# Optimization experiments

Measured on AMD Instinct MI355X. Metric: run time of the kernel, lower is better.

## Reference

```python
import jax, jax.numpy as jnp
import numpy as np

B, S, D, H = 4, 2048, 512, 8
INNER = D  # assumed AttentionHead.inner_size == size (naive single-head attention)


def setup_inputs() -> dict:
    key = jax.random.key(0)
    ks = jax.random.split(key, 8)
    scale = 0.02
    return {
        "emb_input": jax.random.normal(ks[0], (B, S, D), dtype=jnp.float32),
        "Wq": jax.random.normal(ks[1], (H, D, INNER), dtype=jnp.float32) * scale,
        "bq": jnp.zeros((H, INNER), dtype=jnp.float32),
        "Wk": jax.random.normal(ks[2], (H, D, INNER), dtype=jnp.float32) * scale,
        "bk": jnp.zeros((H, INNER), dtype=jnp.float32),
        "Wv": jax.random.normal(ks[3], (H, D, INNER), dtype=jnp.float32) * scale,
        "bv": jnp.zeros((H, INNER), dtype=jnp.float32),
        "Wp": jax.random.normal(ks[4], (H * INNER, D), dtype=jnp.float32) * scale,
        "bp": jnp.zeros((D,), dtype=jnp.float32),
    }


def reference(emb_input, Wq, bq, Wk, bk, Wv, bv, Wp, bp):
    # All heads batched into one einsum instead of a Python loop over submodules.
    x = emb_input  # [B, S, D]
    q = jnp.einsum("bsd,hde->bhse", x, Wq) + bq[None, :, None, :]  # [B,H,S,E]
    k = jnp.einsum("bsd,hde->bhse", x, Wk) + bk[None, :, None, :]
    v = jnp.einsum("bsd,hde->bhse", x, Wv) + bv[None, :, None, :]
    scores = jnp.einsum("bhse,bhte->bhst", q, k) / jnp.sqrt(
        jnp.asarray(INNER, dtype=x.dtype)
    )  # [B,H,S,S]
    attn = jax.nn.softmax(scores, axis=-1)
    o = jnp.einsum("bhst,bhte->bhse", attn, v)  # [B,H,S,E]
    # concat over heads (dim=2 in torch => feature dim after per-head outputs)
    o = jnp.transpose(o, (0, 2, 1, 3)).reshape(B, S, H * INNER)
    return o @ Wp + bp  # [B, S, D]
```

## Files before the change

kernel.cpp:

```cpp
#include <hip/hip_runtime.h>


typedef short s8v __attribute__((ext_vector_type(8)));
typedef float f4v __attribute__((ext_vector_type(4)));
typedef unsigned short us;
typedef us us4v __attribute__((ext_vector_type(4)));

__device__ inline us f2b(float f) {
  union { float f; unsigned u; } v; v.f = f;
  unsigned r = v.u + 0x7FFFu + ((v.u >> 16) & 1u);
  return (us)(r >> 16);
}

__device__ inline void gld16(const us* g, us* l) {
  __builtin_amdgcn_global_load_lds(
      (const __attribute__((address_space(1))) void*)g,
      (__attribute__((address_space(3))) void*)l, 16, 0, 0);
}

__global__ __launch_bounds__(512, 2) void attn_fused(
    const us* __restrict__ Q, const us* __restrict__ Kh,
    const us* __restrict__ Vt, us* __restrict__ O,
    int Lh, float alpha) {
  constexpr int S = 2048, E = 512;
  constexpr int NCH = (S / 128) * 8;
  __shared__ __align__(16) us smem[66560];
  const int t = threadIdx.x, w = t >> 6, ln = t & 63;
  const int m16 = ln & 15, quad = ln >> 4;

  const int gx = gridDim.x;
  const int nblk = gx * gridDim.y;
  const int flat = blockIdx.x + gx * blockIdx.y;
  int nid = flat;
  if ((nblk & 7) == 0) nid = (flat & 7) * (nblk >> 3) + (flat >> 3);
  const int qt = nid % gx, zh = nid / gx;

  const long long zoff = (long long)zh * S * E;
  const us* Qz = Q + zoff;
  const us* Kz = Kh + zoff;
  const us* Vz = Vt + zoff;
  const int q0 = qt * 128;

  s8v Qf[16];
  {
    const us* qrow = Qz + (long long)(q0 + 16 * w + m16) * E + quad * 8;
#pragma unroll
    for (int kq = 0; kq < 16; ++kq) Qf[kq] = *(const s8v*)(qrow + kq * 32);
  }

  f4v accO[4][8];
#pragma unroll
  for (int e = 0; e < 4; ++e)
#pragma unroll
    for (int nb = 0; nb < 8; ++nb) accO[e][nb] = (f4v){0.f, 0.f, 0.f, 0.f};
  float la[4] = {0.f, 0.f, 0.f, 0.f};

#define STAGE(g_, sl_)                                                       \
  {                                                                          \
    const int tau_ = (g_) >> 3, sub_ = (g_) & 7;                             \
    us* dst_ = smem + (sl_) * 16384;                                         \
    _Pragma("unroll") for (int j = 0; j < 4; ++j) {                          \
      const int c_ = t + 512 * j;                                            \
      const int s_ = c_ >> 6, l_ = c_ & 63;                                  \
      const int nbm_ = ((s_ >> 2) * 16 + (l_ & 15));                         \
      const int kk_ = (s_ & 3) * 32 + (l_ >> 4) * 8;                         \
      const us* src_ = (sub_ < 4)                                            \
          ? Kz + (long long)(tau_ * 128 + nbm_) * E + sub_ * 128 + kk_       \
          : Vz + (long long)((sub_ - 4) * 128 + nbm_) * S + tau_ * 128 + kk_;\
      gld16(src_, dst_ + c_ * 8);                                            \
    }                                                                        \
  }

  STAGE(0, 0);
  STAGE(1, 1);
  STAGE(2, 2);
  int sl = 0;

  for (int tau = 0; tau < S / 128; ++tau) {
    f4v accS[8];
#pragma unroll
    for (int nb = 0; nb < 8; ++nb) accS[nb] = (f4v){0.f, 0.f, 0.f, 0.f};
    s8v pa[4];
#pragma unroll
    for (int ph = 0; ph < 8; ++ph) {
      const int g = tau * 8 + ph;
      const int slc = sl;
      if (g + 3 <= NCH)      asm volatile("s_waitcnt vmcnt(8)" ::: "memory");
      else if (g + 2 == NCH) asm volatile("s_waitcnt vmcnt(4)" ::: "memory");
      else                   asm volatile("s_waitcnt vmcnt(0)" ::: "memory");
      __builtin_amdgcn_s_barrier();
      const us* rb = smem + slc * 16384;
      __builtin_amdgcn_s_setprio(1);
#pragma unroll
      for (int ks = 0; ks < 4; ++ks) {
#pragma unroll
        for (int h = 0; h < 2; ++h) {
          s8v bf[4];
#pragma unroll
          for (int nb = 0; nb < 4; ++nb)
            bf[nb] = *(const s8v*)&rb[(((h * 4 + nb) * 4 + ks) * 64 + ln) * 8];
          if (ph < 4) {
#pragma unroll
            for (int nb = 0; nb < 4; ++nb)
              accS[h * 4 + nb] = __builtin_amdgcn_mfma_f32_16x16x32_bf16(
                  Qf[ph * 4 + ks], bf[nb], accS[h * 4 + nb], 0, 0, 0);
          } else {
#pragma unroll
            for (int nb = 0; nb < 4; ++nb)
              accO[ph - 4][h * 4 + nb] = __builtin_amdgcn_mfma_f32_16x16x32_bf16(
                  pa[ks], bf[nb], accO[ph - 4][h * 4 + nb], 0, 0, 0);
          }
        }
      }
      __builtin_amdgcn_s_setprio(0);
      __builtin_amdgcn_s_barrier();
      if (g + 3 < NCH) STAGE(g + 3, slc);
      if (ph == 3) {
        us* pw = smem + 49152 + w * 2176;
#pragma unroll
        for (int nb = 0; nb < 8; ++nb)
#pragma unroll
          for (int gg = 0; gg < 4; ++gg) {
            accS[nb][gg] = __expf(fmaf(accS[nb][gg], alpha, -4.f));
            pw[(quad * 4 + gg) * 136 + nb * 16 + m16] = f2b(accS[nb][gg]);
          }
#pragma unroll
        for (int gg = 0; gg < 4; ++gg) {
          float s = 0.f;
#pragma unroll
          for (int nb = 0; nb < 8; ++nb) s += accS[nb][gg];
          s += __shfl_xor(s, 1, 64);
          s += __shfl_xor(s, 2, 64);
          s += __shfl_xor(s, 4, 64);
          s += __shfl_xor(s, 8, 64);
          la[gg] += s;
        }
        asm volatile("s_waitcnt lgkmcnt(0)" ::: "memory");
        __builtin_amdgcn_sched_barrier(0);
#pragma unroll
        for (int kp = 0; kp < 4; ++kp)
          pa[kp] = *(const s8v*)&pw[m16 * 136 + kp * 32 + quad * 8];
      }
      sl = (slc == 2) ? 0 : slc + 1;
    }
  }
#undef STAGE

  float inv[4];
#pragma unroll
  for (int gg = 0; gg < 4; ++gg) inv[gg] = 1.f / la[gg];
  const int b = zh >> Lh, hc = zh & ((1 << Lh) - 1);
  const int HCE = E << Lh;
  us* Ob = O + (long long)b * S * HCE + (long long)hc * E;
  us* stw = smem + w * 4288;
#pragma unroll
  for (int half = 0; half < 2; ++half) {
#pragma unroll
    for (int ec = 0; ec < 2; ++ec) {
      const int ecg = half * 2 + ec;
#pragma unroll
      for (int nb = 0; nb < 8; ++nb)
#pragma unroll
        for (int gg = 0; gg < 4; ++gg)
          stw[(quad * 4 + gg) * 268 + ec * 128 + nb * 16 + m16] =
              f2b(accO[ecg][nb][gg] * inv[gg]);
    }
    asm volatile("s_waitcnt lgkmcnt(0)" ::: "memory");
    __builtin_amdgcn_sched_barrier(0);
#pragma unroll
    for (int rp = 0; rp < 8; ++rp) {
      const int row = rp * 2 + (ln >> 5);
      const s8v v = *(const s8v*)&stw[row * 268 + (ln & 31) * 8];
      __builtin_nontemporal_store(
          v, (s8v*)&Ob[(long long)(q0 + 16 * w + row) * HCE + half * 256 +
                       (ln & 31) * 8]);
    }
    if (half == 0) {
      asm volatile("s_waitcnt lgkmcnt(0)" ::: "memory");
      __builtin_amdgcn_sched_barrier(0);
    }
  }
}

template <int EPI>
__global__ __launch_bounds__(512, 2) void gemm_nt(
    const us* __restrict__ A, int lda, long long sA0, long long sA1,
    const us* __restrict__ Bm, int ldb, long long sB0, long long sB1,
    const float* __restrict__ bias, const float* __restrict__ bias2,
    const float* __restrict__ bias3,
    void* __restrict__ Cv, void* __restrict__ C2, void* __restrict__ C3,
    int ldc, long long sC0, long long sC1,
    int K, float alpha, int L, int sbits) {
  __shared__ __align__(16) us As[2][16384];
  __shared__ __align__(16) us Bs[2][16384];
  const int t = threadIdx.x;
  const int wv = t >> 6, ln = t & 63;
  const int m16 = ln & 15, quad = ln >> 4;

  const int gx = gridDim.x, gxy = gx * gridDim.y;
  const int nblk = gxy * gridDim.z;
  const int flat = blockIdx.x + gx * blockIdx.y + gxy * blockIdx.z;
  int nid = flat;
  if ((nblk & 7) == 0) nid = (flat & 7) * (nblk >> 3) + (flat >> 3);
  const int bz = nid / gxy, rem = nid % gxy;
  const int by = rem / gx, bx = rem % gx;

  const long long row0 = (long long)by * 256;
  const long long col0 = (long long)bx * 256;
  const int zo = bz >> L, zi = bz & ((1 << L) - 1);
  const us* Az = A + zo * sA0 + zi * sA1;
  const us* Bz = Bm + zo * sB0 + zi * sB1;

  int offA[4], offB[4];
#pragma unroll
  for (int j = 0; j < 4; ++j) {
    const int c = t + 512 * j;
    const int s = c >> 6, l = c & 63;
    const int mb = s >> 1, ks = s & 1, qd = (l >> 4) & 3, mm = l & 15;
    offA[j] = (int)((row0 + mb * 16 + mm) * (long long)lda + ks * 32 + qd * 8);
    offB[j] = (int)((col0 + mb * 16 + mm) * (long long)ldb + ks * 32 + qd * 8);
  }

  f4v acc[8][4];
#pragma unroll
  for (int r = 0; r < 8; ++r)
#pragma unroll
    for (int c = 0; c < 4; ++c) acc[r][c] = (f4v){0.f, 0.f, 0.f, 0.f};

  const int nk = K >> 6;
  const int wr = wv >> 2, wc = wv & 3;

#define BARR __builtin_amdgcn_s_barrier()
#define LGKM0                                              \
  do {                                                     \
    asm volatile("s_waitcnt lgkmcnt(0)" ::: "memory");     \
    __builtin_amdgcn_sched_barrier(0);                     \
  } while (0)
#define READ_A(p_)                                                           \
  _Pragma("unroll") for (int rr = 0; rr < 2; ++rr)                           \
  _Pragma("unroll") for (int ks = 0; ks < 2; ++ks)                           \
      af[rr * 2 + ks] = *(const s8v*)&As[b]                                  \
          [(((wr * 8 + (p_) * 2 + rr) * 2 + ks) * 64 + ln) * 8];
#define MFMA_Q(p_)                                                           \
  __builtin_amdgcn_s_setprio(1);                                             \
  _Pragma("unroll") for (int ks = 0; ks < 2; ++ks)                           \
  _Pragma("unroll") for (int rr = 0; rr < 2; ++rr)                           \
  _Pragma("unroll") for (int c = 0; c < 4; ++c)                              \
      acc[(p_) * 2 + rr][c] = __builtin_amdgcn_mfma_f32_16x16x32_bf16(       \
          af[rr * 2 + ks], bfr[c * 2 + ks], acc[(p_) * 2 + rr][c], 0, 0, 0); \
  __builtin_amdgcn_s_setprio(0);

#pragma unroll
  for (int j = 0; j < 4; ++j) gld16(Az + offA[j], (us*)As[0] + (t + 512 * j) * 8);
#pragma unroll
  for (int j = 0; j < 4; ++j) gld16(Bz + offB[j], (us*)Bs[0] + (t + 512 * j) * 8);
  if (nk > 1) {
#pragma unroll
    for (int j = 0; j < 4; ++j)
      gld16(Bz + offB[j] + 64, (us*)Bs[1] + (t + 512 * j) * 8);
    gld16(Az + offA[0] + 64, (us*)As[1] + t * 8);
    gld16(Az + offA[2] + 64, (us*)As[1] + (t + 1024) * 8);
    asm volatile("s_waitcnt vmcnt(6)" ::: "memory");
  } else {
    asm volatile("s_waitcnt vmcnt(0)" ::: "memory");
  }
  BARR;

  for (int kt = 0; kt < nk; ++kt) {
    const int b = kt & 1;
    s8v bfr[8], af[4];
#pragma unroll
    for (int c = 0; c < 4; ++c)
#pragma unroll
      for (int ks = 0; ks < 2; ++ks)
        bfr[c * 2 + ks] =
            *(const s8v*)&Bs[b][(((wc * 4 + c) * 2 + ks) * 64 + ln) * 8];
    READ_A(0);
    if (kt + 1 < nk) {
      const int kof = (kt + 1) << 6;
      gld16(Az + offA[1] + kof, (us*)As[b ^ 1] + (t + 512) * 8);
      gld16(Az + offA[3] + kof, (us*)As[b ^ 1] + (t + 1536) * 8);
    }
    asm volatile("s_waitcnt lgkmcnt(8)" ::: "memory");
    BARR; LGKM0; MFMA_Q(0); BARR;
    READ_A(1);
    if (kt + 2 < nk) {
      const int kof = (kt + 2) << 6;
#pragma unroll
      for (int j = 0; j < 4; ++j)
        gld16(Bz + offB[j] + kof, (us*)Bs[b] + (t + 512 * j) * 8);
    }
    BARR; LGKM0; MFMA_Q(1); BARR;
    READ_A(2);
    if (kt + 2 < nk) {
      const int kof = (kt + 2) << 6;
      gld16(Az + offA[0] + kof, (us*)As[b] + t * 8);
      gld16(Az + offA[2] + kof, (us*)As[b] + (t + 1024) * 8);
    }
    BARR; LGKM0; MFMA_Q(2); BARR;
    READ_A(3);
    BARR; LGKM0; MFMA_Q(3);
    if (kt + 2 < nk) asm volatile("s_waitcnt vmcnt(6)" ::: "memory");
    else             asm volatile("s_waitcnt vmcnt(0)" ::: "memory");
    BARR;
  }
#undef READ_A
#undef MFMA_Q
#undef BARR
#undef LGKM0

#pragma unroll
  for (int r = 0; r < 8; ++r) {
    const int inRow = wr * 128 + r * 16 + quad * 4;
    const long long gr0 = row0 + inRow;
#pragma unroll
    for (int c = 0; c < 4; ++c) {
      const long long gc = col0 + wc * 64 + c * 16 + m16;
      if (EPI == 3) {
        const int which = (int)(gc >> sbits);
        const int gsec = (int)gc & ((1 << sbits) - 1);
        const int hc = gsec >> 9, e = (int)gc & 511;
        const long long slice =
            ((long long)zo * (1 << (sbits - 9)) + hc) * 1048576LL;
        if (which == 0) {
          us* C = (us*)Cv;
          const float bb = bias[gsec];
#pragma unroll
          for (int g = 0; g < 4; ++g)
            __builtin_nontemporal_store(f2b(acc[r][c][g] + bb),
                                        &C[slice + (gr0 + g) * 512 + e]);
        } else if (which == 1) {
          us* C = (us*)C2;
          const float bb = bias2[gsec];
#pragma unroll
          for (int g = 0; g < 4; ++g)
            __builtin_nontemporal_store(f2b(acc[r][c][g] + bb),
                                        &C[slice + (gr0 + g) * 512 + e]);
        } else {
          us* C = (us*)C3;
          const float bb = bias3[gsec];
          us4v pk;
#pragma unroll
          for (int g = 0; g < 4; ++g) pk[g] = f2b(acc[r][c][g] + bb);
          __builtin_nontemporal_store(
              pk, (us4v*)&C[slice + (long long)e * 2048 + gr0]);
        }
      } else {
        float* C = (float*)Cv + zo * sC0;
        float* p = C + gr0 * ldc + gc;
#pragma unroll
        for (int g = 0; g < 4; ++g)
          atomicAdd(&p[(long long)g * ldc], acc[r][c][g] * alpha);
      }
    }
  }
}

__global__ __launch_bounds__(256) void conv_bf16(const float* __restrict__ in,
                                                 us* __restrict__ out, int n4) {
  const int i = blockIdx.x * 256 + threadIdx.x;
  if (i < n4) {
    const float4 f = ((const float4*)in)[i];
    us4v o;
    o[0] = f2b(f.x); o[1] = f2b(f.y); o[2] = f2b(f.z); o[3] = f2b(f.w);
    ((us4v*)out)[i] = o;
  }
}

__global__ __launch_bounds__(256) void conv_transpose(const float* __restrict__ in,
                                                      us* __restrict__ out,
                                                      int R, int C, int Lc,
                                                      int mask, long long sChunk) {
  __shared__ float tile[32][33];
  const int tx = threadIdx.x & 31, ty = threadIdx.x >> 5;
  const int z = blockIdx.z;
  const long long zi = (long long)z * R * C;
  us* dst = out + (long long)(z >> Lc) * sChunk + (long long)(z & mask) * R * C;
  const int r0 = blockIdx.y * 32, c0 = blockIdx.x * 32;
#pragma unroll
  for (int j = 0; j < 4; ++j)
    tile[ty + 8 * j][tx] = in[zi + (long long)(r0 + ty + 8 * j) * C + c0 + tx];
  __syncthreads();
#pragma unroll
  for (int j = 0; j < 4; ++j)
    dst[(long long)(c0 + ty + 8 * j) * R + r0 + tx] = f2b(tile[tx][ty + 8 * j]);
}

__global__ __launch_bounds__(256) void init_out_kernel(float* __restrict__ out,
                                                       const float* __restrict__ bp,
                                                       int total) {
  const int i = blockIdx.x * 256 + threadIdx.x;
  if (i < total) out[i] = bp[i & 511];
}

extern "C" void kernel_launch(void* const* d_in, const int* in_sizes, int n_in,
                              void* d_out, int out_size, void* d_ws, size_t ws_size,
                              hipStream_t stream) {
  constexpr int Bb = 4, S = 2048, D = 512, H = 8, E = 512, HE = 4096;
  const float* x  = (const float*)d_in[0];
  const float* Wq = (const float*)d_in[1];
  const float* bq = (const float*)d_in[2];
  const float* Wk = (const float*)d_in[3];
  const float* bk = (const float*)d_in[4];
  const float* Wv = (const float*)d_in[5];
  const float* bv = (const float*)d_in[6];
  const float* Wp = (const float*)d_in[7];
  const float* bp = (const float*)d_in[8];
  float* out = (float*)d_out;

  const long long SE = (long long)S * E;
  const long long SD = (long long)S * D, ED = (long long)E * D;

  us* xh  = (us*)d_ws;
  us* W3  = xh + 4194304;
  us* WpT = W3 + 6291456;
  us* dyn = WpT + 2097152;

  const size_t fixedB = (size_t)(4194304 + 6291456 + 2097152) * 2;
  int HC = 8;
  while (HC > 1) {
    const size_t need = fixedB + (size_t)4 * HC * Bb * SE * 2;
    if (need <= ws_size) break;
    HC >>= 1;
  }
  const int Lh = (HC == 8) ? 3 : (HC == 4) ? 2 : (HC == 2) ? 1 : 0;
  const int BHC = Bb * HC;
  const int sbits = 9 + Lh;

  us* qh = dyn;
  us* kh = qh + (size_t)BHC * SE;
  us* vT = kh + (size_t)BHC * SE;
  us* oh = vT + (size_t)BHC * SE;

  const dim3 tb(256), tg(512);
  init_out_kernel<<<dim3((Bb * S * D + 255) / 256), tb, 0, stream>>>(
      out, bp, Bb * S * D);
  conv_bf16<<<dim3(4194304 / 4 / 256), tb, 0, stream>>>(x, xh, 4194304 / 4);
  const long long sChunk = 3LL * HC * ED;
  conv_transpose<<<dim3(16, 16, H), tb, 0, stream>>>(Wq, W3, D, E, Lh, HC - 1, sChunk);
  conv_transpose<<<dim3(16, 16, H), tb, 0, stream>>>(Wk, W3 + HC * ED, D, E, Lh, HC - 1, sChunk);
  conv_transpose<<<dim3(16, 16, H), tb, 0, stream>>>(Wv, W3 + 2 * HC * ED, D, E, Lh, HC - 1, sChunk);
  conv_transpose<<<dim3(16, 128, 1), tb, 0, stream>>>(Wp, WpT, HE, D, 0, 0, 0);

  const float aS = 0.044194173824159216f;
  const dim3 gQKV(3 * HC * E / 256, 8, Bb);
  const dim3 gAT(S / 128, BHC);
  const dim3 gOP(2, 8, BHC);

  for (int c = 0; c < H / HC; ++c) {
    const int h0 = c * HC;
    gemm_nt<3><<<gQKV, tg, 0, stream>>>(
        xh, D, SD, 0, W3 + c * sChunk, D, 0, 0,
        bq + h0 * E, bk + h0 * E, bv + h0 * E,
        qh, kh, vT, 512, 0, SE, D, 1.f, 0, sbits);
    attn_fused<<<gAT, tg, 0, stream>>>(qh, kh, vT, oh, Lh, aS);
    gemm_nt<5><<<gOP, tg, 0, stream>>>(
        oh, HC * E, (long long)S * HC * E, 512,
        WpT + (long long)h0 * E, HE, 0, 512,
        nullptr, nullptr, nullptr, out, nullptr, nullptr,
        D, SD, 0, 512, 1.f, Lh, 0);
  }
}
```

Baseline: 1.098 ms.

## Halve attention tile to 64 queries and 64-key blocks with 4-wave workgroups

The fused attention kernel now processes 64 query rows per workgroup of 256 threads instead of 128 rows with 512 threads. Keys are consumed in 64-wide blocks, so the staging layout, the P buffer in shared memory and the MFMA loops are resized. Shared memory per block drops, and twice as many blocks are launched, which should raise occupancy and improve load balance. The cost is twice the K/V traffic per query and more loop iterations with barriers. Separately, nontemporal stores in the attention and QKV GEMM epilogues are replaced by ordinary stores, so the outputs can stay in cache for the next kernel.

```diff
diff --git a/kernel.cpp b/kernel.cpp
--- a/kernel.cpp
+++ b/kernel.cpp
@@ -18,13 +18,13 @@
       (__attribute__((address_space(3))) void*)l, 16, 0, 0);
 }
 
-__global__ __launch_bounds__(512, 2) void attn_fused(
+__global__ __launch_bounds__(256, 2) void attn_fused(
     const us* __restrict__ Q, const us* __restrict__ Kh,
     const us* __restrict__ Vt, us* __restrict__ O,
     int Lh, float alpha) {
   constexpr int S = 2048, E = 512;
-  constexpr int NCH = (S / 128) * 8;
-  __shared__ __align__(16) us smem[66560];
+  constexpr int NCH = (S / 64) * 8;
+  __shared__ __align__(16) us smem[28928];
   const int t = threadIdx.x, w = t >> 6, ln = t & 63;
   const int m16 = ln & 15, quad = ln >> 4;
 
@@ -39,7 +39,7 @@
   const us* Qz = Q + zoff;
   const us* Kz = Kh + zoff;
   const us* Vz = Vt + zoff;
-  const int q0 = qt * 128;
+  const int q0 = qt * 64;
 
   s8v Qf[16];
   {
@@ -58,15 +58,20 @@
 #define STAGE(g_, sl_)                                                       \
   {                                                                          \
     const int tau_ = (g_) >> 3, sub_ = (g_) & 7;                             \
-    us* dst_ = smem + (sl_) * 16384;                                         \
+    us* dst_ = smem + (sl_) * 8192;                                          \
     _Pragma("unroll") for (int j = 0; j < 4; ++j) {                          \
-      const int c_ = t + 512 * j;                                            \
+      const int c_ = t + 256 * j;                                            \
       const int s_ = c_ >> 6, l_ = c_ & 63;                                  \
-      const int nbm_ = ((s_ >> 2) * 16 + (l_ & 15));                         \
-      const int kk_ = (s_ & 3) * 32 + (l_ >> 4) * 8;                         \
-      const us* src_ = (sub_ < 4)                                            \
-          ? Kz + (long long)(tau_ * 128 + nbm_) * E + sub_ * 128 + kk_       \
-          : Vz + (long long)((sub_ - 4) * 128 + nbm_) * S + tau_ * 128 + kk_;\
+      const us* src_;                                                        \
+      if (sub_ < 4) {                                                        \
+        const int nbm_ = (s_ >> 2) * 16 + (l_ & 15);                         \
+        const int kk_ = (s_ & 3) * 32 + (l_ >> 4) * 8;                       \
+        src_ = Kz + (long long)(tau_ * 64 + nbm_) * E + sub_ * 128 + kk_;    \
+      } else {                                                               \
+        const int nbm_ = (s_ >> 1) * 16 + (l_ & 15);                         \
+        const int kk_ = (s_ & 1) * 32 + (l_ >> 4) * 8;                       \
+        src_ = Vz + (long long)((sub_ - 4) * 128 + nbm_) * S + tau_ * 64 + kk_;\
+      }                                                                      \
       gld16(src_, dst_ + c_ * 8);                                            \
     }                                                                        \
   }
@@ -76,11 +81,11 @@
   STAGE(2, 2);
   int sl = 0;
 
-  for (int tau = 0; tau < S / 128; ++tau) {
-    f4v accS[8];
-#pragma unroll
-    for (int nb = 0; nb < 8; ++nb) accS[nb] = (f4v){0.f, 0.f, 0.f, 0.f};
-    s8v pa[4];
+  for (int tau = 0; tau < S / 64; ++tau) {
+    f4v accS[4];
+#pragma unroll
+    for (int nb = 0; nb < 4; ++nb) accS[nb] = (f4v){0.f, 0.f, 0.f, 0.f};
+    s8v pa[2];
 #pragma unroll
     for (int ph = 0; ph < 8; ++ph) {
       const int g = tau * 8 + ph;
@@ -89,26 +94,34 @@
       else if (g + 2 == NCH) asm volatile("s_waitcnt vmcnt(4)" ::: "memory");
       else                   asm volatile("s_waitcnt vmcnt(0)" ::: "memory");
       __builtin_amdgcn_s_barrier();
-      const us* rb = smem + slc * 16384;
+      const us* rb = smem + slc * 8192;
       __builtin_amdgcn_s_setprio(1);
-#pragma unroll
-      for (int ks = 0; ks < 4; ++ks) {
-#pragma unroll
-        for (int h = 0; h < 2; ++h) {
+      if (ph < 4) {
+#pragma unroll
+        for (int ks = 0; ks < 4; ++ks) {
           s8v bf[4];
 #pragma unroll
           for (int nb = 0; nb < 4; ++nb)
-            bf[nb] = *(const s8v*)&rb[(((h * 4 + nb) * 4 + ks) * 64 + ln) * 8];
-          if (ph < 4) {
+            bf[nb] = *(const s8v*)&rb[((nb * 4 + ks) * 64 + ln) * 8];
+#pragma unroll
+          for (int nb = 0; nb < 4; ++nb)
+            accS[nb] = __builtin_amdgcn_mfma_f32_16x16x32_bf16(
+                Qf[ph * 4 + ks], bf[nb], accS[nb], 0, 0, 0);
+        }
+      } else {
+        const int ec = ph - 4;
+#pragma unroll
+        for (int ks = 0; ks < 2; ++ks) {
+#pragma unroll
+          for (int h = 0; h < 2; ++h) {
+            s8v bf[4];
 #pragma unroll
             for (int nb = 0; nb < 4; ++nb)
-              accS[h * 4 + nb] = __builtin_amdgcn_mfma_f32_16x16x32_bf16(
-                  Qf[ph * 4 + ks], bf[nb], accS[h * 4 + nb], 0, 0, 0);
-          } else {
+              bf[nb] = *(const s8v*)&rb[(((h * 4 + nb) * 2 + ks) * 64 + ln) * 8];
 #pragma unroll
             for (int nb = 0; nb < 4; ++nb)
-              accO[ph - 4][h * 4 + nb] = __builtin_amdgcn_mfma_f32_16x16x32_bf16(
-                  pa[ks], bf[nb], accO[ph - 4][h * 4 + nb], 0, 0, 0);
+              accO[ec][h * 4 + nb] = __builtin_amdgcn_mfma_f32_16x16x32_bf16(
+                  pa[ks], bf[nb], accO[ec][h * 4 + nb], 0, 0, 0);
           }
         }
       }
@@ -116,19 +129,17 @@
       __builtin_amdgcn_s_barrier();
       if (g + 3 < NCH) STAGE(g + 3, slc);
       if (ph == 3) {
-        us* pw = smem + 49152 + w * 2176;
-#pragma unroll
-        for (int nb = 0; nb < 8; ++nb)
+        us* pw = smem + 24576 + w * 1088;
+#pragma unroll
+        for (int nb = 0; nb < 4; ++nb)
 #pragma unroll
           for (int gg = 0; gg < 4; ++gg) {
             accS[nb][gg] = __expf(fmaf(accS[nb][gg], alpha, -4.f));
-            pw[(quad * 4 + gg) * 136 + nb * 16 + m16] = f2b(accS[nb][gg]);
+            pw[(quad * 4 + gg) * 68 + nb * 16 + m16] = f2b(accS[nb][gg]);
           }
 #pragma unroll
         for (int gg = 0; gg < 4; ++gg) {
-          float s = 0.f;
-#pragma unroll
-          for (int nb = 0; nb < 8; ++nb) s += accS[nb][gg];
+          float s = accS[0][gg] + accS[1][gg] + accS[2][gg] + accS[3][gg];
           s += __shfl_xor(s, 1, 64);
           s += __shfl_xor(s, 2, 64);
           s += __shfl_xor(s, 4, 64);
@@ -137,9 +148,8 @@
         }
         asm volatile("s_waitcnt lgkmcnt(0)" ::: "memory");
         __builtin_amdgcn_sched_barrier(0);
-#pragma unroll
-        for (int kp = 0; kp < 4; ++kp)
-          pa[kp] = *(const s8v*)&pw[m16 * 136 + kp * 32 + quad * 8];
+        pa[0] = *(const s8v*)&pw[m16 * 68 + quad * 8];
+        pa[1] = *(const s8v*)&pw[m16 * 68 + 32 + quad * 8];
       }
       sl = (slc == 2) ? 0 : slc + 1;
     }
@@ -171,9 +181,8 @@
     for (int rp = 0; rp < 8; ++rp) {
       const int row = rp * 2 + (ln >> 5);
       const s8v v = *(const s8v*)&stw[row * 268 + (ln & 31) * 8];
-      __builtin_nontemporal_store(
-          v, (s8v*)&Ob[(long long)(q0 + 16 * w + row) * HCE + half * 256 +
-                       (ln & 31) * 8]);
+      *(s8v*)&Ob[(long long)(q0 + 16 * w + row) * HCE + half * 256 +
+                 (ln & 31) * 8] = v;
     }
     if (half == 0) {
       asm volatile("s_waitcnt lgkmcnt(0)" ::: "memory");
@@ -327,23 +336,20 @@
           const float bb = bias[gsec];
 #pragma unroll
           for (int g = 0; g < 4; ++g)
-            __builtin_nontemporal_store(f2b(acc[r][c][g] + bb),
-                                        &C[slice + (gr0 + g) * 512 + e]);
+            C[slice + (gr0 + g) * 512 + e] = f2b(acc[r][c][g] + bb);
         } else if (which == 1) {
           us* C = (us*)C2;
           const float bb = bias2[gsec];
 #pragma unroll
           for (int g = 0; g < 4; ++g)
-            __builtin_nontemporal_store(f2b(acc[r][c][g] + bb),
-                                        &C[slice + (gr0 + g) * 512 + e]);
+            C[slice + (gr0 + g) * 512 + e] = f2b(acc[r][c][g] + bb);
         } else {
           us* C = (us*)C3;
           const float bb = bias3[gsec];
           us4v pk;
 #pragma unroll
           for (int g = 0; g < 4; ++g) pk[g] = f2b(acc[r][c][g] + bb);
-          __builtin_nontemporal_store(
-              pk, (us4v*)&C[slice + (long long)e * 2048 + gr0]);
+          *(us4v*)&C[slice + (long long)e * 2048 + gr0] = pk;
         }
       } else {
         float* C = (float*)Cv + zo * sC0;
@@ -444,7 +450,7 @@
 
   const float aS = 0.044194173824159216f;
   const dim3 gQKV(3 * HC * E / 256, 8, Bb);
-  const dim3 gAT(S / 128, BHC);
+  const dim3 gAT(S / 64, BHC);
   const dim3 gOP(2, 8, BHC);
 
   for (int c = 0; c < H / HC; ++c) {
@@ -453,7 +459,7 @@
         xh, D, SD, 0, W3 + c * sChunk, D, 0, 0,
         bq + h0 * E, bk + h0 * E, bv + h0 * E,
         qh, kh, vT, 512, 0, SE, D, 1.f, 0, sbits);
-    attn_fused<<<gAT, tg, 0, stream>>>(qh, kh, vT, oh, Lh, aS);
+    attn_fused<<<gAT, tb, 0, stream>>>(qh, kh, vT, oh, Lh, aS);
     gemm_nt<5><<<gOP, tg, 0, stream>>>(
         oh, HC * E, (long long)S * HC * E, 512,
         WpT + (long long)h0 * E, HE, 0, 512,
```

Measured after the change: 1.094 ms. Within noise of the previous version (-0.4%).
